# Performance work log

Measured on AMD Instinct MI355X. Metric: run time of the kernel, lower is better.

Reference implementation:

```python
import jax, jax.numpy as jnp
import numpy as np

B, T, C, H = 2, 2048, 1024, 16
HD = C // H  # head dim = 64


def setup_inputs() -> dict:
    key = jax.random.key(0)
    k1, k2, k3 = jax.random.split(key, 3)
    scale_in = 1.0 / np.sqrt(C)
    x = jax.random.normal(k1, (B, T, C), dtype=jnp.float32)
    w_qkv = jax.random.normal(k2, (C, 3 * C), dtype=jnp.float32) * scale_in
    b_qkv = jnp.zeros((3 * C,), dtype=jnp.float32)
    w_out = jax.random.normal(k3, (C, C), dtype=jnp.float32) * scale_in
    b_out = jnp.zeros((C,), dtype=jnp.float32)
    return {"x": x, "w_qkv": w_qkv, "b_qkv": b_qkv, "w_out": w_out, "b_out": b_out}


def reference(x, w_qkv, b_qkv, w_out, b_out):
    Bq, Tq, Cq = x.shape
    qkv = x @ w_qkv + b_qkv                       # [B,T,3C]
    q, k, v = jnp.split(qkv, 3, axis=-1)          # each [B,T,C]
    # [B,T,C] -> [B,H,T,HD]
    q = q.reshape(Bq, Tq, H, HD).transpose(0, 2, 1, 3)
    k = k.reshape(Bq, Tq, H, HD).transpose(0, 2, 1, 3)
    v = v.reshape(Bq, Tq, H, HD).transpose(0, 2, 1, 3)
    scale = 1.0 / np.sqrt(HD)
    scores = jnp.einsum("bhqd,bhkd->bhqk", q, k) * scale  # [B,H,T,T]
    causal = jnp.tril(jnp.ones((Tq, Tq), dtype=bool))
    scores = jnp.where(causal[None, None], scores, jnp.finfo(scores.dtype).min)
    attn = jax.nn.softmax(scores, axis=-1)
    y = jnp.einsum("bhqk,bhkd->bhqd", attn, v)    # [B,H,T,HD]
    y = y.transpose(0, 2, 1, 3).reshape(Bq, Tq, Cq)
    return y @ w_out + b_out
```

## Files before the change

### kernel.cpp

```cpp
#include <hip/hip_runtime.h>
#include <hip/hip_bf16.h>


#define B_ 2
#define T_ 2048
#define C_ 1024
#define H_ 16
#define HD_ 64
#define M_ (B_ * T_)
#define N3_ (3 * C_)
#define QK2_ 2048
#define QSCALE 0.18033688f
#define PSTR 76

typedef __attribute__((ext_vector_type(8))) short short8;
typedef __attribute__((ext_vector_type(4))) short short4v;
typedef __attribute__((ext_vector_type(4))) float floatx4;

__device__ __forceinline__ unsigned short f2b(float f) {
    __hip_bfloat16 h = __float2bfloat16(f);
    return *reinterpret_cast<unsigned short*>(&h);
}

__device__ __forceinline__ void glds16(const void* g, void* l) {
    __builtin_amdgcn_global_load_lds(
        (const __attribute__((address_space(1))) void*)g,
        (__attribute__((address_space(3))) void*)l, 16, 0, 0);
}

__global__ __launch_bounds__(256) void prep(
    const float* __restrict__ x, const float* __restrict__ w_qkv,
    const float* __restrict__ w_out, unsigned short* __restrict__ xb,
    unsigned short* __restrict__ wt1, unsigned short* __restrict__ wt2) {
    __shared__ float t[32][33];
    const int bi = blockIdx.x;
    const int tid = threadIdx.x;
    if (bi < 4096) {
        int i = (bi * 256 + tid) * 4;
        float4 v = *reinterpret_cast<const float4*>(x + i);
        short4v s;
        s[0] = (short)f2b(v.x); s[1] = (short)f2b(v.y);
        s[2] = (short)f2b(v.z); s[3] = (short)f2b(v.w);
        *reinterpret_cast<short4v*>(xb + i) = s;
        return;
    }
    const float* src; unsigned short* dst; int n0, k0, N;
    if (bi < 4096 + 3072) {
        int u = bi - 4096;
        src = w_qkv; dst = wt1; N = N3_;
        n0 = (u % 96) * 32; k0 = (u / 96) * 32;
    } else {
        int u = bi - 7168;
        src = w_out; dst = wt2; N = C_;
        n0 = (u & 31) * 32; k0 = (u >> 5) * 32;
    }
    const int tx = tid & 31, ty = tid >> 5;
#pragma unroll
    for (int i = 0; i < 4; i++)
        t[ty + i * 8][tx] = src[(size_t)(k0 + ty + i * 8) * N + n0 + tx];
    __syncthreads();
#pragma unroll
    for (int i = 0; i < 4; i++)
        dst[(size_t)(n0 + ty + i * 8) * C_ + k0 + tx] = f2b(t[tx][ty + i * 8]);
}

template<int EPI, int BN>
__global__ __launch_bounds__(256) void gemm_glds(
    const unsigned short* __restrict__ A, const unsigned short* __restrict__ Bt,
    const float* __restrict__ bias, void* __restrict__ Cp,
    unsigned short* __restrict__ vtp, int M, int N, int K) {
    constexpr int NI = BN / 32;
    __shared__ __align__(16) unsigned short Al[128 * 64];
    __shared__ __align__(16) unsigned short Bl[BN * 64];

    const int tid  = threadIdx.x;
    const int lane = tid & 63;
    const int w    = tid >> 6;
    const int c16  = lane & 15;
    const int quad = lane >> 4;
    const int n0 = blockIdx.x * BN;
    const int m0 = blockIdx.y * 128;
    const int wm = (w >> 1) * 64;
    const int wn = (w & 1) * (BN / 2);

    floatx4 acc[4][NI] = {};

    const int srow = lane >> 3;
    const int sch  = ((lane & 7) ^ srow) * 8;
    const unsigned short* ag = A + (size_t)(m0 + w * 32 + srow) * K + sch;
    const unsigned short* bg = Bt + (size_t)(n0 + w * (BN / 4) + srow) * K + sch;

    const int s7 = c16 & 7;

    for (int k0 = 0; k0 < K; k0 += 64) {
        __syncthreads();
#pragma unroll
        for (int i = 0; i < 4; i++)
            glds16(ag + k0 + (size_t)(i * 8) * K, &Al[(w * 32 + i * 8) * 64]);
#pragma unroll
        for (int i = 0; i < BN / 32; i++)
            glds16(bg + k0 + (size_t)(i * 8) * K,
                   &Bl[(w * (BN / 4) + i * 8) * 64]);
        __syncthreads();

        short8 af[4][2], bf[NI][2];
#pragma unroll
        for (int im = 0; im < 4; im++)
#pragma unroll
            for (int kk = 0; kk < 2; kk++)
                af[im][kk] = *reinterpret_cast<const short8*>(
                    &Al[(wm + im * 16 + c16) * 64 + ((kk * 4 + quad) ^ s7) * 8]);
#pragma unroll
        for (int in = 0; in < NI; in++)
#pragma unroll
            for (int kk = 0; kk < 2; kk++)
                bf[in][kk] = *reinterpret_cast<const short8*>(
                    &Bl[(wn + in * 16 + c16) * 64 + ((kk * 4 + quad) ^ s7) * 8]);
#pragma unroll
        for (int im = 0; im < 4; im++)
#pragma unroll
            for (int in = 0; in < NI; in++)
#pragma unroll
                for (int kk = 0; kk < 2; kk++)
                    acc[im][in] = __builtin_amdgcn_mfma_f32_16x16x32_bf16(
                        af[im][kk], bf[in][kk], acc[im][in], 0, 0, 0);
    }

    const int ncol = n0 + wn;
    float bv[NI];
#pragma unroll
    for (int in = 0; in < NI; in++) bv[in] = bias[ncol + in * 16 + c16];

    if (EPI == 0) {
        float* C = (float*)Cp;
#pragma unroll
        for (int im = 0; im < 4; im++)
#pragma unroll
            for (int r = 0; r < 4; r++) {
                int row = m0 + wm + im * 16 + quad * 4 + r;
#pragma unroll
                for (int in = 0; in < NI; in++)
                    C[(size_t)row * N + ncol + in * 16 + c16] =
                        acc[im][in][r] + bv[in];
            }
    } else {
        if (ncol < 2 * C_) {
            const float fac = (ncol < C_) ? QSCALE : 1.0f;
            unsigned short* qkp = (unsigned short*)Cp;
#pragma unroll
            for (int im = 0; im < 4; im++)
#pragma unroll
                for (int r = 0; r < 4; r++) {
                    int row = m0 + wm + im * 16 + quad * 4 + r;
#pragma unroll
                    for (int in = 0; in < NI; in++)
                        qkp[(size_t)row * QK2_ + ncol + in * 16 + c16] =
                            f2b((acc[im][in][r] + bv[in]) * fac);
                }
        } else {
#pragma unroll
            for (int im = 0; im < 4; im++) {
                int row0 = m0 + wm + im * 16 + quad * 4;
                int b  = row0 >> 11;
                int t0 = row0 & (T_ - 1);
#pragma unroll
                for (int in = 0; in < NI; in++) {
                    int dfull = ncol - 2 * C_ + in * 16 + c16;
                    short4v sv;
#pragma unroll
                    for (int r = 0; r < 4; r++)
                        sv[r] = (short)f2b(acc[im][in][r] + bv[in]);
                    *reinterpret_cast<short4v*>(
                        &vtp[(((size_t)(b << 10) + dfull) << 11) + t0]) = sv;
                }
            }
        }
    }
}

template<bool MASKED>
__device__ __forceinline__ void attn_tile(
    short8 af0, short8 af1,
    const unsigned short* __restrict__ Kl,
    const unsigned short* __restrict__ Vl,
    unsigned short* __restrict__ pw,
    floatx4 O[4], float& l,
    int row0, int kb, int c16, int quad) {
    const floatx4 z = {0.f, 0.f, 0.f, 0.f};
    const int sx  = c16 & 7;
    const int ch0 = (quad ^ sx) * 8;
    const int ch1 = ((quad + 4) ^ sx) * 8;
    floatx4 s[4];
#pragma unroll
    for (int nt = 0; nt < 4; nt++) {
        const int rb = (nt * 16 + c16) * 64;
        short8 k0 = *reinterpret_cast<const short8*>(&Kl[rb + ch0]);
        short8 k1 = *reinterpret_cast<const short8*>(&Kl[rb + ch1]);
        floatx4 t = __builtin_amdgcn_mfma_f32_16x16x32_bf16(k0, af0, z, 0, 0, 0);
        s[nt] = __builtin_amdgcn_mfma_f32_16x16x32_bf16(k1, af1, t, 0, 0, 0);
    }
    const int qrow = row0 + c16;
#pragma unroll
    for (int nt = 0; nt < 4; nt++) {
        short4v p4;
#pragma unroll
        for (int r = 0; r < 4; r++) {
            float p;
            if (MASKED) {
                int key = kb + nt * 16 + quad * 4 + r;
                p = (key <= qrow) ? exp2f(s[nt][r]) : 0.f;
            } else {
                p = exp2f(s[nt][r]);
            }
            l += p;
            p4[r] = (short)f2b(p);
        }
        *reinterpret_cast<short4v*>(&pw[c16 * PSTR + nt * 16 + quad * 4]) = p4;
    }
    short8 pf0 = *reinterpret_cast<const short8*>(&pw[c16 * PSTR + quad * 8]);
    short8 pf1 = *reinterpret_cast<const short8*>(&pw[c16 * PSTR + 32 + quad * 8]);
#pragma unroll
    for (int nt = 0; nt < 4; nt++) {
        const int rb = (nt * 16 + c16) * 64;
        short8 v0 = *reinterpret_cast<const short8*>(&Vl[rb + ch0]);
        short8 v1 = *reinterpret_cast<const short8*>(&Vl[rb + ch1]);
        floatx4 t = __builtin_amdgcn_mfma_f32_16x16x32_bf16(pf0, v0, O[nt], 0, 0, 0);
        O[nt] = __builtin_amdgcn_mfma_f32_16x16x32_bf16(pf1, v1, t, 0, 0, 0);
    }
}

__global__ __launch_bounds__(256) void attn_mfma(
    const unsigned short* __restrict__ qk,
    const unsigned short* __restrict__ vt,
    unsigned short* __restrict__ y) {
    __shared__ __align__(16) unsigned short Kl[64 * 64];
    __shared__ __align__(16) unsigned short Vl[64 * 64];
    __shared__ __align__(16) unsigned short Pl[4 * 16 * PSTR];

    const int tid  = threadIdx.x;
    const int lane = tid & 63;
    const int w    = tid >> 6;
    const int c16  = lane & 15;
    const int quad = lane >> 4;
    const int bh = blockIdx.x & 31;
    const int t  = 31 - (blockIdx.x >> 5);
    const int b  = bh >> 4;
    const int h  = bh & 15;
    const int row0 = (4 * t + w) * 16;
    const int nch  = t + 1;

    const unsigned short* qrow = qk + (size_t)b * T_ * QK2_ + h * HD_;
    const unsigned short* krow = qrow + C_;
    const unsigned short* vrow = vt + ((size_t)bh << 6) * T_;

    short8 af0 = *reinterpret_cast<const short8*>(
        qrow + (size_t)(row0 + c16) * QK2_ + quad * 8);
    short8 af1 = *reinterpret_cast<const short8*>(
        qrow + (size_t)(row0 + c16) * QK2_ + 32 + quad * 8);

    floatx4 O[4] = {};
    float l = 0.f;
    unsigned short* pw = &Pl[w * 16 * PSTR];

    const int r8 = lane >> 3;
    const int sw = ((lane & 7) ^ r8) * 8;

    for (int c = 0; c < nch; c++) {
        const int kb = c * 64;
        __syncthreads();
#pragma unroll
        for (int i = 0; i < 2; i++) {
            const int row = w * 16 + i * 8 + r8;
            glds16(krow + (size_t)(kb + row) * QK2_ + sw,
                   &Kl[(w * 16 + i * 8) * 64]);
            glds16(vrow + (size_t)row * T_ + kb + sw,
                   &Vl[(w * 16 + i * 8) * 64]);
        }
        __syncthreads();

        if (c + 1 < nch)
            attn_tile<false>(af0, af1, Kl, Vl, pw, O, l, row0, kb, c16, quad);
        else
            attn_tile<true>(af0, af1, Kl, Vl, pw, O, l, row0, kb, c16, quad);
    }

    l += __shfl_xor(l, 16);
    l += __shfl_xor(l, 32);
    float lr[4];
#pragma unroll
    for (int r = 0; r < 4; r++)
        lr[r] = __shfl(l, quad * 4 + r);

#pragma unroll
    for (int nt = 0; nt < 4; nt++)
#pragma unroll
        for (int r = 0; r < 4; r++) {
            float val = O[nt][r] / fmaxf(lr[r], 1e-30f);
            y[((size_t)b * T_ + row0 + quad * 4 + r) * C_ + h * HD_ + nt * 16 + c16] =
                f2b(val);
        }
}

extern "C" void kernel_launch(void* const* d_in, const int* in_sizes, int n_in,
                              void* d_out, int out_size, void* d_ws, size_t ws_size,
                              hipStream_t stream) {
    const float* x     = (const float*)d_in[0];
    const float* w_qkv = (const float*)d_in[1];
    const float* b_qkv = (const float*)d_in[2];
    const float* w_out = (const float*)d_in[3];
    const float* b_out = (const float*)d_in[4];
    float* out = (float*)d_out;

    unsigned short* qkb = (unsigned short*)d_ws;
    unsigned short* vtb = qkb + (size_t)M_ * QK2_;
    unsigned short* yb  = vtb + (size_t)B_ * H_ * HD_ * T_;
    unsigned short* wt1 = yb + (size_t)M_ * C_;
    unsigned short* wt2 = wt1 + (size_t)N3_ * C_;
    unsigned short* xb  = wt2 + (size_t)C_ * C_;

    prep<<<4096 + 3072 + 1024, 256, 0, stream>>>(x, w_qkv, w_out, xb, wt1, wt2);

    dim3 g1(N3_ / 128, M_ / 128);
    gemm_glds<1, 128><<<g1, 256, 0, stream>>>(xb, wt1, b_qkv, qkb, vtb, M_, N3_, C_);

    attn_mfma<<<B_ * H_ * 32, 256, 0, stream>>>(qkb, vtb, yb);

    dim3 g2(C_ / 64, M_ / 128);
    gemm_glds<0, 64><<<g2, 256, 0, stream>>>(yb, wt2, b_out, out, nullptr, M_, C_, C_);
}
```

Before: 188.1 us.

## Double-buffer K/V tiles in LDS and swizzle the P scratch layout

New measurement: 179.5 us. 1.05x faster.

```diff
diff --git a/kernel.cpp b/kernel.cpp
--- a/kernel.cpp
+++ b/kernel.cpp
@@ -11,7 +11,6 @@
 #define N3_ (3 * C_)
 #define QK2_ 2048
 #define QSCALE 0.18033688f
-#define PSTR 76
 
 typedef __attribute__((ext_vector_type(8))) short short8;
 typedef __attribute__((ext_vector_type(4))) short short4v;
@@ -181,8 +180,8 @@
 template<bool MASKED>
 __device__ __forceinline__ void attn_tile(
     short8 af0, short8 af1,
-    const unsigned short* __restrict__ Kl,
-    const unsigned short* __restrict__ Vl,
+    const unsigned short* __restrict__ Kb,
+    const unsigned short* __restrict__ Vb,
     unsigned short* __restrict__ pw,
     floatx4 O[4], float& l,
     int row0, int kb, int c16, int quad) {
@@ -194,8 +193,8 @@
 #pragma unroll
     for (int nt = 0; nt < 4; nt++) {
         const int rb = (nt * 16 + c16) * 64;
-        short8 k0 = *reinterpret_cast<const short8*>(&Kl[rb + ch0]);
-        short8 k1 = *reinterpret_cast<const short8*>(&Kl[rb + ch1]);
+        short8 k0 = *reinterpret_cast<const short8*>(&Kb[rb + ch0]);
+        short8 k1 = *reinterpret_cast<const short8*>(&Kb[rb + ch1]);
         floatx4 t = __builtin_amdgcn_mfma_f32_16x16x32_bf16(k0, af0, z, 0, 0, 0);
         s[nt] = __builtin_amdgcn_mfma_f32_16x16x32_bf16(k1, af1, t, 0, 0, 0);
     }
@@ -215,15 +214,16 @@
             l += p;
             p4[r] = (short)f2b(p);
         }
-        *reinterpret_cast<short4v*>(&pw[c16 * PSTR + nt * 16 + quad * 4]) = p4;
-    }
-    short8 pf0 = *reinterpret_cast<const short8*>(&pw[c16 * PSTR + quad * 8]);
-    short8 pf1 = *reinterpret_cast<const short8*>(&pw[c16 * PSTR + 32 + quad * 8]);
+        const int pst = ((2 * nt + (quad >> 1)) ^ sx) * 8 + (quad & 1) * 4;
+        *reinterpret_cast<short4v*>(&pw[c16 * 64 + pst]) = p4;
+    }
+    short8 pf0 = *reinterpret_cast<const short8*>(&pw[c16 * 64 + ch0]);
+    short8 pf1 = *reinterpret_cast<const short8*>(&pw[c16 * 64 + ch1]);
 #pragma unroll
     for (int nt = 0; nt < 4; nt++) {
         const int rb = (nt * 16 + c16) * 64;
-        short8 v0 = *reinterpret_cast<const short8*>(&Vl[rb + ch0]);
-        short8 v1 = *reinterpret_cast<const short8*>(&Vl[rb + ch1]);
+        short8 v0 = *reinterpret_cast<const short8*>(&Vb[rb + ch0]);
+        short8 v1 = *reinterpret_cast<const short8*>(&Vb[rb + ch1]);
         floatx4 t = __builtin_amdgcn_mfma_f32_16x16x32_bf16(pf0, v0, O[nt], 0, 0, 0);
         O[nt] = __builtin_amdgcn_mfma_f32_16x16x32_bf16(pf1, v1, t, 0, 0, 0);
     }
@@ -233,9 +233,9 @@
     const unsigned short* __restrict__ qk,
     const unsigned short* __restrict__ vt,
     unsigned short* __restrict__ y) {
-    __shared__ __align__(16) unsigned short Kl[64 * 64];
-    __shared__ __align__(16) unsigned short Vl[64 * 64];
-    __shared__ __align__(16) unsigned short Pl[4 * 16 * PSTR];
+    __shared__ __align__(16) unsigned short Kl[2][64 * 64];
+    __shared__ __align__(16) unsigned short Vl[2][64 * 64];
+    __shared__ __align__(16) unsigned short Pl[4 * 16 * 64];
 
     const int tid  = threadIdx.x;
     const int lane = tid & 63;
@@ -260,28 +260,39 @@
 
     floatx4 O[4] = {};
     float l = 0.f;
-    unsigned short* pw = &Pl[w * 16 * PSTR];
+    unsigned short* pw = &Pl[w * 16 * 64];
 
     const int r8 = lane >> 3;
     const int sw = ((lane & 7) ^ r8) * 8;
 
+#pragma unroll
+    for (int i = 0; i < 2; i++) {
+        const int row = w * 16 + i * 8 + r8;
+        glds16(krow + (size_t)row * QK2_ + sw, &Kl[0][(w * 16 + i * 8) * 64]);
+        glds16(vrow + (size_t)row * T_ + sw,   &Vl[0][(w * 16 + i * 8) * 64]);
+    }
+
     for (int c = 0; c < nch; c++) {
+        __syncthreads();
+        if (c + 1 < nch) {
+            const int kb2 = (c + 1) * 64;
+            const int nb = (c + 1) & 1;
+#pragma unroll
+            for (int i = 0; i < 2; i++) {
+                const int row = w * 16 + i * 8 + r8;
+                glds16(krow + (size_t)(kb2 + row) * QK2_ + sw,
+                       &Kl[nb][(w * 16 + i * 8) * 64]);
+                glds16(vrow + (size_t)row * T_ + kb2 + sw,
+                       &Vl[nb][(w * 16 + i * 8) * 64]);
+            }
+        }
         const int kb = c * 64;
-        __syncthreads();
-#pragma unroll
-        for (int i = 0; i < 2; i++) {
-            const int row = w * 16 + i * 8 + r8;
-            glds16(krow + (size_t)(kb + row) * QK2_ + sw,
-                   &Kl[(w * 16 + i * 8) * 64]);
-            glds16(vrow + (size_t)row * T_ + kb + sw,
-                   &Vl[(w * 16 + i * 8) * 64]);
-        }
-        __syncthreads();
-
         if (c + 1 < nch)
-            attn_tile<false>(af0, af1, Kl, Vl, pw, O, l, row0, kb, c16, quad);
+            attn_tile<false>(af0, af1, Kl[c & 1], Vl[c & 1], pw, O, l,
+                             row0, kb, c16, quad);
         else
-            attn_tile<true>(af0, af1, Kl, Vl, pw, O, l, row0, kb, c16, quad);
+            attn_tile<true>(af0, af1, Kl[c & 1], Vl[c & 1], pw, O, l,
+                            row0, kb, c16, quad);
     }
 
     l += __shfl_xor(l, 16);
```
